# Kernel optimization log

Measured on AMD Instinct MI355X. Metric: run time of the kernel, lower is better.

## Reference

```python
import jax, jax.numpy as jnp
import numpy as np

N, C, W, H = 16, 64, 512, 512
RED, OUT_W = 64, 128
BN_EPS = 1e-5


def setup_inputs() -> dict:
    key = jax.random.key(0)
    ks = jax.random.split(key, 5)
    x = jax.random.normal(ks[0], (N, C, W, H), dtype=jnp.float32)
    w1 = jax.random.normal(ks[1], (RED, W), dtype=jnp.float32) * (1.0 / np.sqrt(W))
    b1 = jax.random.normal(ks[2], (RED,), dtype=jnp.float32) * 0.01
    gamma = jnp.ones((RED,), dtype=jnp.float32)
    beta = jnp.zeros((RED,), dtype=jnp.float32)
    w2 = jax.random.normal(ks[3], (W, RED), dtype=jnp.float32) * (1.0 / np.sqrt(RED))
    b2 = jax.random.normal(ks[4], (W,), dtype=jnp.float32) * 0.01
    return {"x": x, "w1": w1, "b1": b1, "gamma": gamma, "beta": beta, "w2": w2, "b2": b2}


def reference(x, w1, b1, gamma, beta, w2, b2):
    # attention_dim == 2: permute(0,2,1,3) -> [N,W,C,H]; AdaptiveMaxPool2d((1,1))
    # over (C,H) == global max over axes (1,3) of original x -> [N, W]
    pooled = jnp.max(x, axis=(1, 3))                       # [N, W]
    # Linear(W -> RED)
    h = pooled @ w1.T + b1                                 # [N, RED]
    # BatchNorm1d in training mode: batch stats (biased variance)
    mu = jnp.mean(h, axis=0)
    var = jnp.mean((h - mu) ** 2, axis=0)
    h = gamma * (h - mu) * jax.lax.rsqrt(var + BN_EPS) + beta
    h = jax.nn.relu(h)
    # Linear(RED -> W) + softmax over width
    att = jax.nn.softmax(h @ w2.T + b2, axis=1)            # [N, W]
    # topk over width, then sort selected indices ascending
    _, idx = jax.lax.top_k(att, OUT_W)                     # [N, OUT_W]
    idx = jnp.sort(idx, axis=1)
    # batched gather along width axis: x[i, :, idx[i], :]
    return jnp.take_along_axis(x, idx[:, None, :, None], axis=2)  # [N, C, OUT_W, H]
```

## Files before the change

kernel.cpp:

```cpp
#include <hip/hip_runtime.h>
#include <cstdint>
#include <math.h>

#define Nn   16
#define Cc   64
#define Ww   512
#define Hh   512
#define RED  64
#define OUTW 128

__global__ void __launch_bounds__(256) pool_kernel(const float* __restrict__ x,
                                                   float* __restrict__ pooled) {
    const int b = blockIdx.x;
    const int n = b >> 7;
    const int q = b & 127;
    const int r = threadIdx.x >> 6;
    const int lane = threadIdx.x & 63;
    const int w = q * 4 + r;
    const float* base = x + ((size_t)n * Cc * Ww + w) * Hh + lane * 8;

    float m0 = -INFINITY, m1 = -INFINITY, m2 = -INFINITY, m3 = -INFINITY;
    float m4 = -INFINITY, m5 = -INFINITY, m6 = -INFINITY, m7 = -INFINITY;
    #pragma unroll 4
    for (int c = 0; c < Cc; ++c) {
        const float* p = base + (size_t)c * (Ww * Hh);
        const float4 v0 = *reinterpret_cast<const float4*>(p);
        const float4 v1 = *reinterpret_cast<const float4*>(p + 4);
        m0 = fmaxf(m0, v0.x); m1 = fmaxf(m1, v0.y);
        m2 = fmaxf(m2, v0.z); m3 = fmaxf(m3, v0.w);
        m4 = fmaxf(m4, v1.x); m5 = fmaxf(m5, v1.y);
        m6 = fmaxf(m6, v1.z); m7 = fmaxf(m7, v1.w);
    }
    float m = fmaxf(fmaxf(fmaxf(m0, m1), fmaxf(m2, m3)),
                    fmaxf(fmaxf(m4, m5), fmaxf(m6, m7)));
    #pragma unroll
    for (int off = 1; off < 64; off <<= 1)
        m = fmaxf(m, __shfl_xor(m, off, 64));
    if (lane == 0) pooled[n * Ww + w] = m;
}

__global__ void __launch_bounds__(256) mlp_h_kernel(
    const float* __restrict__ pooled,
    const float* __restrict__ w1,
    const float* __restrict__ b1,
    const float* __restrict__ gamma,
    const float* __restrict__ beta,
    float* __restrict__ hbn)
{
    const int r = blockIdx.x;
    const int t = threadIdx.x;
    const int n = t & 15;
    const int slice = t >> 4;
    const float4* w1r = reinterpret_cast<const float4*>(w1 + r * Ww + slice * 32);
    const float4* pn  = reinterpret_cast<const float4*>(pooled + n * Ww + slice * 32);

    float acc = 0.f;
    #pragma unroll
    for (int j = 0; j < 8; ++j) {
        const float4 a = w1r[j];
        const float4 p = pn[j];
        acc += a.x * p.x + a.y * p.y + a.z * p.z + a.w * p.w;
    }
    __shared__ float part[16][17];
    part[slice][n] = acc;
    __syncthreads();
    if (t < 16) {
        float h = b1[r];
        #pragma unroll
        for (int s = 0; s < 16; ++s) h += part[s][t];
        float sum = h, sq = h * h;
        #pragma unroll
        for (int off = 1; off < 16; off <<= 1) {
            sum += __shfl_xor(sum, off, 64);
            sq  += __shfl_xor(sq,  off, 64);
        }
        const float mu  = sum * (1.f / 16.f);
        const float var = sq  * (1.f / 16.f) - mu * mu;
        const float is  = 1.f / sqrtf(var + 1e-5f);
        const float v   = gamma[r] * (h - mu) * is + beta[r];
        hbn[r * Nn + t] = fmaxf(v, 0.f);
    }
}

__global__ void __launch_bounds__(512) logits_topk_kernel(
    const float* __restrict__ hbn,
    const float* __restrict__ w2,
    const float* __restrict__ b2,
    int* __restrict__ idx_out)
{
    const int row = blockIdx.x;
    const int w = threadIdx.x;

    __shared__ float hrow[RED];
    __shared__ float logits_row[Ww];
    __shared__ unsigned long long sel_mask[Ww / 64];

    float4 wv[16];
    const float4* w2r = reinterpret_cast<const float4*>(w2 + w * RED);
    #pragma unroll
    for (int j = 0; j < 16; ++j) wv[j] = w2r[j];
    if (w < RED) hrow[w] = hbn[w * Nn + row];
    __syncthreads();

    float acc = b2[w];
    #pragma unroll
    for (int j = 0; j < 16; ++j) {
        acc += wv[j].x * hrow[j * 4]     + wv[j].y * hrow[j * 4 + 1]
             + wv[j].z * hrow[j * 4 + 2] + wv[j].w * hrow[j * 4 + 3];
    }
    logits_row[w] = acc;
    __syncthreads();

    const float v = logits_row[w];
    int rank = 0;
    for (int ww = 0; ww < Ww; ++ww) {
        const float u = logits_row[ww];
        rank += (u > v || (u == v && ww < w)) ? 1 : 0;
    }
    const bool sel = (rank < OUTW);
    const unsigned long long m = __ballot(sel);
    if ((w & 63) == 0) sel_mask[w >> 6] = m;
    __syncthreads();
    if (sel) {
        int pos = 0;
        #pragma unroll
        for (int bb = 0; bb < (Ww / 64); ++bb)
            if (bb < (w >> 6)) pos += __popcll(sel_mask[bb]);
        pos += __popcll(sel_mask[w >> 6] & ((1ULL << (w & 63)) - 1ULL));
        idx_out[row * OUTW + pos] = w;
    }
}

__global__ void __launch_bounds__(256) gather_kernel(const float* __restrict__ x,
                                                     const int* __restrict__ idx,
                                                     float* __restrict__ out) {
    const int b = blockIdx.x;
    const int n = b >> 6;
    const int tid = threadIdx.x;
    __shared__ int sidx[OUTW];
    if (tid < OUTW) sidx[tid] = idx[n * OUTW + tid];
    __syncthreads();
    const float* src = x   + (size_t)b * (Ww * Hh);
    float*       dst = out + (size_t)b * (OUTW * Hh);
    #pragma unroll 4
    for (int i = tid; i < OUTW * (Hh / 4); i += 256) {
        const int j = i >> 7;
        const int f = i & 127;
        const float4 v = *reinterpret_cast<const float4*>(src + (size_t)sidx[j] * Hh + f * 4);
        *reinterpret_cast<float4*>(dst + (size_t)j * Hh + f * 4) = v;
    }
}

extern "C" void kernel_launch(void* const* d_in, const int* in_sizes, int n_in,
                              void* d_out, int out_size, void* d_ws, size_t ws_size,
                              hipStream_t stream) {
    const float* x     = (const float*)d_in[0];
    const float* w1    = (const float*)d_in[1];
    const float* b1    = (const float*)d_in[2];
    const float* gamma = (const float*)d_in[3];
    const float* beta  = (const float*)d_in[4];
    const float* w2    = (const float*)d_in[5];
    const float* b2    = (const float*)d_in[6];
    float* out = (float*)d_out;

    float* pooled = (float*)d_ws;
    float* hbn    = (float*)((char*)d_ws + 32768);
    int*   idx    = (int*)((char*)d_ws + 32768 + 4096);

    pool_kernel<<<Nn * (Ww / 4), 256, 0, stream>>>(x, pooled);
    mlp_h_kernel<<<RED, 256, 0, stream>>>(pooled, w1, b1, gamma, beta, hbn);
    logits_topk_kernel<<<Nn, 512, 0, stream>>>(hbn, w2, b2, idx);
    gather_kernel<<<Nn * Cc, 256, 0, stream>>>(x, idx, out);
}
```

Before: 323.0 us.

## Split max-pool into per-plane contiguous partial max plus channel reduction

Replaces the channel-strided pooling kernel with one that reads each (n,c) plane contiguously and computes per-row maxima over H via shared memory, followed by a small kernel reducing over channels. The intent is more sequential DRAM access for the dominant 1 GB read. It adds an extra launch, a workspace buffer, and heavy LDS use that may limit occupancy; it falls back to the old kernel if workspace is too small.

```diff
diff --git a/kernel.cpp b/kernel.cpp
--- a/kernel.cpp
+++ b/kernel.cpp
@@ -8,6 +8,47 @@
 #define Hh   512
 #define RED  64
 #define OUTW 128
+
+__global__ void __launch_bounds__(256) pool_partial_kernel(
+    const float* __restrict__ x, float* __restrict__ partial) {
+    const int b = blockIdx.x;
+    const float* plane = x + (size_t)b * (Ww * Hh);
+    const int wv = threadIdx.x >> 6;
+    const int lane = threadIdx.x & 63;
+    __shared__ float part[128][65];
+
+    for (int k = 0; k < 4; ++k) {
+        #pragma unroll 4
+        for (int i = 0; i < 32; ++i) {
+            const int rl = i * 4 + wv;
+            const float* p = plane + (size_t)(k * 128 + rl) * Hh + lane * 8;
+            const float4 v0 = *reinterpret_cast<const float4*>(p);
+            const float4 v1 = *reinterpret_cast<const float4*>(p + 4);
+            const float m = fmaxf(fmaxf(fmaxf(v0.x, v0.y), fmaxf(v0.z, v0.w)),
+                                  fmaxf(fmaxf(v1.x, v1.y), fmaxf(v1.z, v1.w)));
+            part[rl][lane] = m;
+        }
+        __syncthreads();
+        if (threadIdx.x < 128) {
+            float m = -INFINITY;
+            #pragma unroll
+            for (int j = 0; j < 64; ++j) m = fmaxf(m, part[threadIdx.x][j]);
+            partial[(size_t)b * Ww + k * 128 + threadIdx.x] = m;
+        }
+        __syncthreads();
+    }
+}
+
+__global__ void __launch_bounds__(256) reduce_c_kernel(
+    const float* __restrict__ partial, float* __restrict__ pooled) {
+    const int o = blockIdx.x * 256 + threadIdx.x;
+    const int n = o >> 9, w = o & 511;
+    float m = -INFINITY;
+    #pragma unroll 8
+    for (int c = 0; c < Cc; ++c)
+        m = fmaxf(m, partial[((size_t)(n * Cc + c)) * Ww + w]);
+    pooled[o] = m;
+}
 
 __global__ void __launch_bounds__(256) pool_kernel(const float* __restrict__ x,
                                                    float* __restrict__ pooled) {
@@ -166,8 +207,15 @@
     float* pooled = (float*)d_ws;
     float* hbn    = (float*)((char*)d_ws + 32768);
     int*   idx    = (int*)((char*)d_ws + 32768 + 4096);
-
-    pool_kernel<<<Nn * (Ww / 4), 256, 0, stream>>>(x, pooled);
+    float* partial= (float*)((char*)d_ws + 65536);
+
+    const size_t need = 65536 + (size_t)Nn * Cc * Ww * sizeof(float);
+    if (ws_size >= need) {
+        pool_partial_kernel<<<Nn * Cc, 256, 0, stream>>>(x, partial);
+        reduce_c_kernel<<<(Nn * Ww) / 256, 256, 0, stream>>>(partial, pooled);
+    } else {
+        pool_kernel<<<Nn * (Ww / 4), 256, 0, stream>>>(x, pooled);
+    }
     mlp_h_kernel<<<RED, 256, 0, stream>>>(pooled, w1, b1, gamma, beta, hbn);
     logits_topk_kernel<<<Nn, 512, 0, stream>>>(hbn, w2, b2, idx);
     gather_kernel<<<Nn * Cc, 256, 0, stream>>>(x, idx, out);
```

Result: slower. 341.5 us (+5.7%).
